# Kernel tuning notes

Measured on AMD Instinct MI355X. Metric: run time of the kernel, lower is better.

Reference implementation:

```python
import jax, jax.numpy as jnp
import numpy as np

B, H, W, P, DEPTH = 128, 512, 512, 64, 4
EPS = 1e-5


def _std(t):
    # torch.std default: unbiased (ddof=1), over last two dims, keepdim
    m = t.mean(axis=(-2, -1), keepdims=True)
    n = t.shape[-1] * t.shape[-2]
    var = ((t - m) ** 2).sum(axis=(-2, -1), keepdims=True) / (n - 1)
    return jnp.sqrt(var)


def _flat_softmax(t):
    # softmax over all non-batch dims (flatten(1).softmax(1).reshape)
    b = t.shape[0]
    return jax.nn.softmax(t.reshape(b, -1), axis=1).reshape(t.shape)


def setup_inputs() -> dict:
    key = jax.random.key(0)
    ks = jax.random.split(key, 9)
    # xavier-uniform-like scale for [*, fan_in, fan_out] params
    def init(k, shape):
        fan_in, fan_out = shape[-2], shape[-1]
        gain = float(np.sqrt(2.0))  # relu gain
        bound = gain * float(np.sqrt(6.0 / (fan_in + fan_out)))
        return jax.random.uniform(k, shape, jnp.float32, -bound, bound)
    return {
        "x": jax.random.normal(ks[0], (B, H, W), jnp.float32),
        "o_xj": init(ks[1], (DEPTH, W, P)),
        "o_xi": init(ks[2], (DEPTH, H, P)),
        "p_xj": init(ks[3], (DEPTH, H, P)),
        "p_xi": init(ks[4], (DEPTH, W, P)),
        "o_rel_xj": init(ks[5], (DEPTH, W, P)),
        "o_rel_xi": init(ks[6], (DEPTH, H, P)),
        "p_rel_xj": init(ks[7], (DEPTH, P, P)),
        "p_rel_xi": init(ks[8], (DEPTH, P, P)),
    }


def reference(x, o_xj, o_xi, p_xj, p_xi, o_rel_xj, o_rel_xi, p_rel_xj, p_rel_xi):
    # eval-mode forward (dropout inactive)
    b, h, w = x.shape
    p = o_xj.shape[-1]
    depth = o_xj.shape[0]
    scale = (h / p) * (w / p)
    x_mean = x.mean(axis=(-2, -1), keepdims=True) * scale  # [B,1,1]
    x_std = _std(x) * scale                                 # [B,1,1]
    xt = jnp.swapaxes(x, -1, -2)                            # [B,W,H]

    projection = jnp.zeros((b, p, p), jnp.float32)
    for d in range(depth):
        # relevance branches on original orientation
        o_rel_xj_sum = _flat_softmax(x @ o_rel_xj[d]).sum(axis=-2)   # [B,P]
        o_rel_xi_sum = _flat_softmax(xt @ o_rel_xi[d]).sum(axis=-2)  # [B,P]
        # projection branches
        o_t_xj = x @ o_xj[d]                                # [B,H,P]
        o_t_xi = xt @ o_xi[d]                               # [B,W,P]
        p_t_xj = jnp.swapaxes(o_t_xj, -1, -2) @ p_xj[d]     # [B,P,P]
        p_t_xi = jnp.swapaxes(o_t_xi, -1, -2) @ p_xi[d]     # [B,P,P]
        # relevance branches on permuted projection
        p_rel_xj_sum = _flat_softmax(p_t_xj @ p_rel_xj[d]).sum(axis=-2)  # [B,P]
        p_rel_xi_sum = _flat_softmax(p_t_xi @ p_rel_xi[d]).sum(axis=-2)  # [B,P]
        f_j = jnp.sqrt(o_rel_xj_sum / p_rel_xj_sum)         # [B,P]
        f_i = jnp.sqrt(o_rel_xi_sum / p_rel_xi_sum)         # [B,P]
        x_buf = p_t_xj * f_j[..., None] + jnp.swapaxes(p_t_xi * f_i[..., None], -1, -2)
        # renormalize to original (scaled) statistics
        x_buf = (x_buf - x_buf.mean(axis=(-2, -1), keepdims=True)) / (_std(x_buf) + EPS)
        x_buf = x_buf * x_std + x_mean
        projection = projection + x_buf
    return projection
```

## Files before the change

kernel.cpp:

```cpp
#include <hip/hip_runtime.h>
#include <math.h>

typedef __attribute__((ext_vector_type(8))) short short8;
typedef __attribute__((ext_vector_type(4))) short short4v;
typedef __attribute__((ext_vector_type(4))) float f32x4;

#define EPSF 1e-5f

__device__ __forceinline__ short f2bf(float f) {
    union { float f; unsigned u; } v; v.f = f;
    unsigned r = (v.u + 0x7FFFu + ((v.u >> 16) & 1u)) >> 16;
    return (short)r;
}

__device__ __forceinline__ void gload16(const void* g, void* l) {
    __builtin_amdgcn_global_load_lds(
        (const __attribute__((address_space(1))) unsigned int*)g,
        (__attribute__((address_space(3))) unsigned int*)l, 16, 0, 0);
}

__global__ __launch_bounds__(256) void prep_kernel(
    const float* __restrict__ x,
    const float* __restrict__ o_xj, const float* __restrict__ o_xi,
    const float* __restrict__ p_xj, const float* __restrict__ p_xi,
    const float* __restrict__ o_rel_xj, const float* __restrict__ o_rel_xi,
    short* __restrict__ xbf, short* __restrict__ xtbf,
    double* __restrict__ part, short* __restrict__ wcat, short* __restrict__ wpt) {
    int tid = threadIdx.x;
    if (blockIdx.x < 4096) {
        int blk = blockIdx.x;
        int b = blk >> 5, R = blk & 31;
        const float* X = x + (size_t)b * 262144 + (size_t)R * 16 * 512;
        __shared__ __align__(16) float tile[16 * 512];
        __shared__ double wsum[4][2];
        int w = tid >> 6, l = tid & 63, li = l & 15, lg = l >> 4;

        #pragma unroll
        for (int ii = 0; ii < 8; ii++) {
            int s = w * 8 + ii;
            gload16(X + s * 256 + l * 4, tile + s * 256);
        }
        __syncthreads();

        double s = 0.0, sq = 0.0;
        #pragma unroll
        for (int q = 0; q < 4; q++) {
            int kt = w * 4 + q;
            const float* p0 = tile + li * 512 + kt * 32 + lg * 8;
            float4 f0 = *(const float4*)p0;
            float4 f1 = *(const float4*)(p0 + 4);
            short v[8];
            v[0] = f2bf(f0.x); v[1] = f2bf(f0.y); v[2] = f2bf(f0.z); v[3] = f2bf(f0.w);
            v[4] = f2bf(f1.x); v[5] = f2bf(f1.y); v[6] = f2bf(f1.z); v[7] = f2bf(f1.w);
            s += (double)f0.x + (double)f0.y + (double)f0.z + (double)f0.w
               + (double)f1.x + (double)f1.y + (double)f1.z + (double)f1.w;
            sq += (double)f0.x * f0.x + (double)f0.y * f0.y + (double)f0.z * f0.z + (double)f0.w * f0.w
                + (double)f1.x * f1.x + (double)f1.y * f1.y + (double)f1.z * f1.z + (double)f1.w * f1.w;
            size_t chunk = (size_t)((b * 32 + R) * 16 + kt);
            *(short8*)(xbf + chunk * 512 + l * 8) = *(const short8*)v;
        }

        int base_lg = (R & 1) * 2;
        int kt2 = R >> 1;
        int lh = l & 31, li2 = lh & 15, lgo = lh >> 4;
        #pragma unroll
        for (int q = 0; q < 4; q++) {
            int p = w * 8 + q * 2 + (l >> 5);
            short v[8];
            #pragma unroll
            for (int e = 0; e < 8; e++)
                v[e] = f2bf(tile[(lgo * 8 + e) * 512 + p * 16 + li2]);
            size_t chunk = (size_t)((b * 32 + p) * 16 + kt2);
            *(short8*)(xtbf + chunk * 512 + (base_lg + lgo) * 128 + li2 * 8) = *(const short8*)v;
        }

        #pragma unroll
        for (int off = 1; off < 64; off <<= 1) {
            s += __shfl_xor(s, off, 64);
            sq += __shfl_xor(sq, off, 64);
        }
        if (l == 0) { wsum[w][0] = s; wsum[w][1] = sq; }
        __syncthreads();
        if (tid == 0) {
            double ts = wsum[0][0] + wsum[1][0] + wsum[2][0] + wsum[3][0];
            double tq = wsum[0][1] + wsum[1][1] + wsum[2][1] + wsum[3][1];
            part[blk * 2] = ts; part[blk * 2 + 1] = tq;
        }
    } else {
        int idx = (blockIdx.x - 4096) * 256 + tid;
        if (idx < 65536) {
            int l = idx & 63; int chunk = idx >> 6;
            int kt = chunk & 15, ns = (chunk >> 4) & 7, sd = chunk >> 7;
            int side = sd >> 2, dd = sd & 3;
            int n = ns * 16 + (l & 15);
            int k = kt * 32 + (l >> 4) * 8;
            const float* src = (n < 64) ? (side ? o_rel_xi : o_rel_xj)
                                        : (side ? o_xi : o_xj);
            src += (size_t)dd * 32768 + (n & 63);
            short8 v;
            #pragma unroll
            for (int e = 0; e < 8; e++) v[e] = f2bf(src[(size_t)(k + e) * 64]);
            *(short8*)(wcat + (size_t)chunk * 512 + l * 8) = v;
        } else {
            int j = idx - 65536;
            int l = j & 63; int chunk = j >> 6;
            int nq = chunk & 3, kk = (chunk >> 2) & 3, mt = (chunk >> 4) & 3, sd = chunk >> 6;
            int side = sd >> 2, dd = sd & 3;
            int q = nq * 16 + (l & 15);
            int r = mt * 128 + kk * 32 + (l >> 4) * 8;
            const float* src = (side ? p_xi : p_xj) + (size_t)dd * 32768 + q;
            short8 v;
            #pragma unroll
            for (int e = 0; e < 8; e++) v[e] = f2bf(src[(size_t)(r + e) * 64]);
            *(short8*)(wpt + (size_t)chunk * 512 + l * 8) = v;
        }
    }
}

__global__ __launch_bounds__(256) void stats_p1(const float* __restrict__ x,
                                                double* __restrict__ part) {
    int blk = blockIdx.x;
    const float4* X = (const float4*)(x + (size_t)blk * 65536);
    double s = 0.0, sq = 0.0;
    for (int i = threadIdx.x; i < 16384; i += 256) {
        float4 v = X[i];
        s += (double)v.x + (double)v.y + (double)v.z + (double)v.w;
        sq += (double)v.x * v.x + (double)v.y * v.y + (double)v.z * v.z + (double)v.w * v.w;
    }
    __shared__ double rs[256], rq[256];
    rs[threadIdx.x] = s; rq[threadIdx.x] = sq;
    __syncthreads();
    for (int st = 128; st > 0; st >>= 1) {
        if (threadIdx.x < st) { rs[threadIdx.x] += rs[threadIdx.x + st]; rq[threadIdx.x] += rq[threadIdx.x + st]; }
        __syncthreads();
    }
    if (threadIdx.x == 0) { part[blk * 2] = rs[0]; part[blk * 2 + 1] = rq[0]; }
}

__global__ void stats_p2(const double* __restrict__ part, float* __restrict__ stats, int ppb) {
    int b = threadIdx.x;
    double s = 0.0, sq = 0.0;
    for (int p = 0; p < ppb; p++) { s += part[(b * ppb + p) * 2]; sq += part[(b * ppb + p) * 2 + 1]; }
    double n = 262144.0;
    double mean = s / n;
    double var = (sq - n * mean * mean) / (n - 1.0);
    stats[b * 2 + 0] = (float)(mean * 64.0);
    stats[b * 2 + 1] = (float)(sqrt(var) * 64.0);
}

__global__ __launch_bounds__(256, 4) void main_mfma_kernel(
    const short* __restrict__ xbf, const short* __restrict__ xtbf,
    const short* __restrict__ wcat, const short* __restrict__ wpt,
    float* __restrict__ relsum, float* __restrict__ pt) {
    int blk = blockIdx.x;
    int xcd = blk & 7, rest = blk >> 3;
    int d = rest & 3, side = (rest >> 2) & 1, bhi = rest >> 3;
    int b = bhi * 8 + xcd;
    const short* Xsw = (side ? xtbf : xbf) + (size_t)b * 262144;
    const short* Wc  = wcat + (size_t)(side * 4 + d) * 65536;
    const short* Wp  = wpt + (size_t)(side * 4 + d) * 32768;

    __shared__ __align__(16) char lds[33792];
    short* Xs  = (short*)lds;
    short* Wsh = (short*)(lds + 8192);
    short* Tos = (short*)lds;
    short* Wps = (short*)(lds + 17408);

    int tid = threadIdx.x;
    int w = tid >> 6, l = tid & 63, li = l & 15, lg = l >> 4;
    int wm = w >> 1, wn = w & 1;

    f32x4 zero4 = {0.f, 0.f, 0.f, 0.f};
    f32x4 ptacc[4];
    #pragma unroll
    for (int i = 0; i < 4; i++) ptacc[i] = zero4;
    float esum[4] = {0.f, 0.f, 0.f, 0.f};

    for (int mt = 0; mt < 4; mt++) {
        f32x4 acc[4][4];
        #pragma unroll
        for (int i = 0; i < 4; i++)
            #pragma unroll
            for (int j = 0; j < 4; j++) acc[i][j] = zero4;

        for (int kt = 0; kt < 16; kt++) {
            __syncthreads();
            #pragma unroll
            for (int ii = 0; ii < 4; ii++) {
                int s = w * 4 + ii;
                if (s < 8)
                    gload16(Xsw + ((size_t)((mt * 8 + s) * 16 + kt)) * 512 + l * 8, Xs + s * 512);
                else
                    gload16(Wc + ((size_t)((s - 8) * 16 + kt)) * 512 + l * 8, Wsh + (s - 8) * 512);
            }
            __syncthreads();
            short8 af[4], bfv[4];
            #pragma unroll
            for (int i = 0; i < 4; i++) af[i] = *(const short8*)(Xs + (wm * 4 + i) * 512 + l * 8);
            #pragma unroll
            for (int j = 0; j < 4; j++) bfv[j] = *(const short8*)(Wsh + (wn * 4 + j) * 512 + l * 8);
            #pragma unroll
            for (int i = 0; i < 4; i++)
                #pragma unroll
                for (int j = 0; j < 4; j++)
                    acc[i][j] = __builtin_amdgcn_mfma_f32_16x16x32_bf16(af[i], bfv[j], acc[i][j], 0, 0, 0);
        }

        #pragma unroll
        for (int ii = 0; ii < 4; ii++) {
            int s = w * 4 + ii;
            gload16(Wp + ((size_t)((mt * 4 + (s >> 2)) * 4 + (s & 3))) * 512 + l * 8, Wps + s * 512);
        }
        __syncthreads();

        if (wn == 0) {
            #pragma unroll
            for (int i = 0; i < 4; i++)
                #pragma unroll
                for (int j = 0; j < 4; j++)
                    esum[j] += __expf(acc[i][j][0]) + __expf(acc[i][j][1]) +
                               __expf(acc[i][j][2]) + __expf(acc[i][j][3]);
        } else {
            #pragma unroll
            for (int i = 0; i < 4; i++)
                #pragma unroll
                for (int j = 0; j < 4; j++) {
                    int p = j * 16 + li;
                    int rb = wm * 64 + i * 16 + lg * 4;
                    short4v tv;
                    tv.x = f2bf(acc[i][j][0]); tv.y = f2bf(acc[i][j][1]);
                    tv.z = f2bf(acc[i][j][2]); tv.w = f2bf(acc[i][j][3]);
                    *(short4v*)(Tos + p * 136 + rb) = tv;
                }
        }
        __syncthreads();

        #pragma unroll
        for (int kk = 0; kk < 4; kk++) {
            short8 a = *(const short8*)(Tos + (w * 16 + li) * 136 + kk * 32 + lg * 8);
            #pragma unroll
            for (int nq = 0; nq < 4; nq++) {
                short8 bb = *(const short8*)(Wps + (kk * 4 + nq) * 512 + l * 8);
                ptacc[nq] = __builtin_amdgcn_mfma_f32_16x16x32_bf16(a, bb, ptacc[nq], 0, 0, 0);
            }
        }
    }

    __syncthreads();
    float* red = (float*)lds;
    if (wn == 0) {
        #pragma unroll
        for (int j = 0; j < 4; j++) red[wm * 256 + l * 4 + j] = esum[j];
    }
    __syncthreads();
    size_t base = (size_t)(b * 2 + side) * 4 + d;
    if (tid < 64) {
        float s = 0.f;
        #pragma unroll
        for (int w2 = 0; w2 < 2; w2++)
            #pragma unroll
            for (int g = 0; g < 4; g++)
                s += red[w2 * 256 + (g * 16 + (tid & 15)) * 4 + (tid >> 4)];
        float tot = s;
        #pragma unroll
        for (int off = 1; off < 64; off <<= 1) tot += __shfl_xor(tot, off, 64);
        relsum[base * 64 + tid] = s / tot;
    }
    float* ptout = pt + base * 4096;
    #pragma unroll
    for (int nq = 0; nq < 4; nq++)
        #pragma unroll
        for (int r = 0; r < 4; r++)
            ptout[(size_t)(w * 16 + lg * 4 + r) * 64 + nq * 16 + li] = ptacc[nq][r];
}

__global__ __launch_bounds__(256) void fused_proj_kernel(
    const float* __restrict__ x,
    const float* __restrict__ o_xj, const float* __restrict__ o_xi,
    const float* __restrict__ p_xj, const float* __restrict__ p_xi,
    const float* __restrict__ o_rel_xj, const float* __restrict__ o_rel_xi,
    float* __restrict__ relsum, float* __restrict__ pt)
{
    int blk = blockIdx.x;
    int b = blk >> 3;
    int side = (blk >> 2) & 1;
    int d = blk & 3;

    const float* Wrel = (side ? o_rel_xi : o_rel_xj) + (size_t)d * (512 * 64);
    const float* Wo   = (side ? o_xi     : o_xj)     + (size_t)d * (512 * 64);
    const float* Wp   = (side ? p_xi     : p_xj)     + (size_t)d * (512 * 64);
    const float* X = x + (size_t)b * (512 * 512);

    __shared__ float Xs[16][68];
    __shared__ float Ws[16][128];
    __shared__ float To[64][68];
    __shared__ float Wps[64][68];
    __shared__ float red[16][64];
    __shared__ float cs[64];
    __shared__ float total_s;

    int tid = threadIdx.x;
    int tx = tid & 15;
    int ty = tid >> 4;

    float paccum[4][4];
    #pragma unroll
    for (int i = 0; i < 4; i++)
        #pragma unroll
        for (int j = 0; j < 4; j++) paccum[i][j] = 0.f;
    float esum[8];
    #pragma unroll
    for (int j = 0; j < 8; j++) esum[j] = 0.f;

    for (int r0 = 0; r0 < 512; r0 += 64) {
        float acc[4][8];
        #pragma unroll
        for (int i = 0; i < 4; i++)
            #pragma unroll
            for (int j = 0; j < 8; j++) acc[i][j] = 0.f;

        for (int k0 = 0; k0 < 512; k0 += 16) {
            if (side == 0) {
                int kk = tid & 15, r = tid >> 4;
                #pragma unroll
                for (int it = 0; it < 4; it++, r += 16)
                    Xs[kk][r] = X[(size_t)(r0 + r) * 512 + (k0 + kk)];
            } else {
                int r = tid & 63, kk = tid >> 6;
                #pragma unroll
                for (int it = 0; it < 4; it++, kk += 4)
                    Xs[kk][r] = X[(size_t)(k0 + kk) * 512 + (r0 + r)];
            }
            {
                int c = tid & 127, kk = tid >> 7;
                const float* Wsrc = (c < 64) ? (Wrel + c) : (Wo + (c - 64));
                #pragma unroll
                for (int it = 0; it < 8; it++, kk += 2)
                    Ws[kk][c] = Wsrc[(size_t)(k0 + kk) * 64];
            }
            __syncthreads();
            #pragma unroll
            for (int kk = 0; kk < 16; kk++) {
                float4 a  = *(const float4*)&Xs[kk][ty * 4];
                float4 b0 = *(const float4*)&Ws[kk][tx * 8];
                float4 b1 = *(const float4*)&Ws[kk][tx * 8 + 4];
                float av[4] = {a.x, a.y, a.z, a.w};
                float bv[8] = {b0.x, b0.y, b0.z, b0.w, b1.x, b1.y, b1.z, b1.w};
                #pragma unroll
                for (int i = 0; i < 4; i++)
                    #pragma unroll
                    for (int j = 0; j < 8; j++)
                        acc[i][j] = fmaf(av[i], bv[j], acc[i][j]);
            }
            __syncthreads();
        }

        if (tx < 8) {
            #pragma unroll
            for (int i = 0; i < 4; i++)
                #pragma unroll
                for (int j = 0; j < 8; j++)
                    esum[j] += expf(acc[i][j]);
        } else {
            #pragma unroll
            for (int i = 0; i < 4; i++) {
                float4 v0 = make_float4(acc[i][0], acc[i][1], acc[i][2], acc[i][3]);
                float4 v1 = make_float4(acc[i][4], acc[i][5], acc[i][6], acc[i][7]);
                *(float4*)&To[ty * 4 + i][(tx - 8) * 8]     = v0;
                *(float4*)&To[ty * 4 + i][(tx - 8) * 8 + 4] = v1;
            }
        }
        {
            int q = tid & 63, r = tid >> 6;
            #pragma unroll
            for (int it = 0; it < 16; it++, r += 4)
                Wps[r][q] = Wp[(size_t)(r0 + r) * 64 + q];
        }
        __syncthreads();
        for (int r = 0; r < 64; r++) {
            float4 aa = *(const float4*)&To[r][ty * 4];
            float4 bb = *(const float4*)&Wps[r][tx * 4];
            float av[4] = {aa.x, aa.y, aa.z, aa.w};
            float bv[4] = {bb.x, bb.y, bb.z, bb.w};
            #pragma unroll
            for (int i = 0; i < 4; i++)
                #pragma unroll
                for (int j = 0; j < 4; j++)
                    paccum[i][j] = fmaf(av[i], bv[j], paccum[i][j]);
        }
        __syncthreads();
    }

    if (tx < 8) {
        #pragma unroll
        for (int j = 0; j < 8; j++) red[ty][tx * 8 + j] = esum[j];
    }
    __syncthreads();
    if (tid < 64) {
        float s = 0.f;
        for (int t = 0; t < 16; t++) s += red[t][tid];
        cs[tid] = s;
    }
    __syncthreads();
    if (tid == 0) {
        float tot = 0.f;
        for (int i = 0; i < 64; i++) tot += cs[i];
        total_s = tot;
    }
    __syncthreads();
    size_t base = (size_t)(b * 2 + side) * 4 + d;
    if (tid < 64) relsum[base * 64 + tid] = cs[tid] / total_s;

    float* ptout = pt + base * 4096;
    #pragma unroll
    for (int i = 0; i < 4; i++)
        #pragma unroll
        for (int j = 0; j < 4; j++)
            ptout[(size_t)(ty * 4 + i) * 64 + tx * 4 + j] = paccum[i][j];
}

__global__ __launch_bounds__(256) void finalize2_kernel(
    const float* __restrict__ relsum, const float* __restrict__ pt,
    const float* __restrict__ p_rel_xj, const float* __restrict__ p_rel_xi,
    const double* __restrict__ part, const float* __restrict__ stats, int ppb,
    float* __restrict__ out)
{
    int blk = blockIdx.x;
    int b = blk >> 2, d = blk & 3;
    int tid = threadIdx.x, tx = tid & 15, ty = tid >> 4;
    __shared__ __align__(16) float Ptj[64][68], Pti[64][68], Wr[64][68];
    __shared__ float red[16][64];
    __shared__ float fj[64], fi[64];
    __shared__ float rs[256], rq[256];
    __shared__ float bc[1];
    __shared__ float sstat[2];

    if (ppb > 0) {
        if (tid < ppb) {
            double s = part[(size_t)(b * ppb + tid) * 2];
            double sq = part[(size_t)(b * ppb + tid) * 2 + 1];
            for (int off = 1; off < ppb; off <<= 1) {
                s += __shfl_xor(s, off, 64);
                sq += __shfl_xor(sq, off, 64);
            }
            if (tid == 0) {
                double n = 262144.0;
                double mean = s / n;
                double var = (sq - n * mean * mean) / (n - 1.0);
                sstat[0] = (float)(mean * 64.0);
                sstat[1] = (float)(sqrt(var) * 64.0);
            }
        }
    } else if (tid == 0) {
        sstat[0] = stats[b * 2 + 0];
        sstat[1] = stats[b * 2 + 1];
    }

    const float* ptj = pt + ((size_t)(b * 2 + 0) * 4 + d) * 4096;
    const float* pti = pt + ((size_t)(b * 2 + 1) * 4 + d) * 4096;
    for (int it = 0; it < 16; it++) {
        int idx = tid + it * 256;
        Ptj[idx >> 6][idx & 63] = ptj[idx];
        Pti[idx >> 6][idx & 63] = pti[idx];
    }
    __syncthreads();
    float x_mean = sstat[0];
    float x_std  = sstat[1];

    for (int s = 0; s < 2; s++) {
        const float* prel = (s == 0) ? (p_rel_xj + (size_t)d * 4096)
                                     : (p_rel_xi + (size_t)d * 4096);
        for (int it = 0; it < 16; it++) {
            int idx = tid + it * 256;
            Wr[idx >> 6][idx & 63] = prel[idx];
        }
        __syncthreads();
        const float (*Pt)[68] = (s == 0) ? Ptj : Pti;
        float q[4][4];
        #pragma unroll
        for (int i = 0; i < 4; i++)
            #pragma unroll
            for (int j = 0; j < 4; j++) q[i][j] = 0.f;
        for (int r = 0; r < 64; r++) {
            float4 bv = *(const float4*)&Wr[r][tx * 4];
            #pragma unroll
            for (int i = 0; i < 4; i++) {
                float a = Pt[ty * 4 + i][r];
                q[i][0] = fmaf(a, bv.x, q[i][0]);
                q[i][1] = fmaf(a, bv.y, q[i][1]);
                q[i][2] = fmaf(a, bv.z, q[i][2]);
                q[i][3] = fmaf(a, bv.w, q[i][3]);
            }
        }
        float cpart[4];
        #pragma unroll
        for (int j = 0; j < 4; j++)
            cpart[j] = __expf(q[0][j]) + __expf(q[1][j]) + __expf(q[2][j]) + __expf(q[3][j]);
        #pragma unroll
        for (int j = 0; j < 4; j++) red[ty][tx * 4 + j] = cpart[j];
        __syncthreads();
        float* ftgt = (s == 0) ? fj : fi;
        if (tid < 64) {
            float cssum = 0.f;
            for (int t = 0; t < 16; t++) cssum += red[t][tid];
            ftgt[tid] = cssum;
        }
        __syncthreads();
        if (tid == 0) {
            float tot = 0.f;
            for (int i = 0; i < 64; i++) tot += ftgt[i];
            bc[0] = tot;
        }
        __syncthreads();
        if (tid < 64) {
            float prel_sum = ftgt[tid] / bc[0];
            float orel = relsum[((size_t)(b * 2 + s) * 4 + d) * 64 + tid];
            ftgt[tid] = sqrtf(orel / prel_sum);
        }
        __syncthreads();
    }

    float v[4][4];
    float psum = 0.f, psq = 0.f;
    #pragma unroll
    for (int i = 0; i < 4; i++) {
        int r = ty * 4 + i;
        #pragma unroll
        for (int j = 0; j < 4; j++) {
            int c = tx * 4 + j;
            float val = Ptj[r][c] * fj[r] + Pti[c][r] * fi[c];
            v[i][j] = val; psum += val; psq += val * val;
        }
    }
    rs[tid] = psum; rq[tid] = psq;
    __syncthreads();
    for (int st = 128; st > 0; st >>= 1) {
        if (tid < st) { rs[tid] += rs[tid + st]; rq[tid] += rq[tid + st]; }
        __syncthreads();
    }
    float mean = rs[0] / 4096.f;
    float var = (rq[0] - 4096.f * mean * mean) / 4095.f;
    float inv = 1.0f / (sqrtf(var) + EPSF);
    float* ob = out + (size_t)b * 4096;
    #pragma unroll
    for (int i = 0; i < 4; i++)
        #pragma unroll
        for (int j = 0; j < 4; j++)
            atomicAdd(&ob[(size_t)(ty * 4 + i) * 64 + tx * 4 + j],
                      (v[i][j] - mean) * inv * x_std + x_mean);
}

extern "C" void kernel_launch(void* const* d_in, const int* in_sizes, int n_in,
                              void* d_out, int out_size, void* d_ws, size_t ws_size,
                              hipStream_t stream) {
    const float* x        = (const float*)d_in[0];
    const float* o_xj     = (const float*)d_in[1];
    const float* o_xi     = (const float*)d_in[2];
    const float* p_xj     = (const float*)d_in[3];
    const float* p_xi     = (const float*)d_in[4];
    const float* o_rel_xj = (const float*)d_in[5];
    const float* o_rel_xi = (const float*)d_in[6];
    const float* p_rel_xj = (const float*)d_in[7];
    const float* p_rel_xi = (const float*)d_in[8];
    float* out = (float*)d_out;

    char* ws = (char*)d_ws;
    float*  stats  = (float*)(ws + 0);
    float*  relsum = (float*)(ws + 1024);
    float*  pt     = (float*)(ws + 263168);
    double* spartF = (double*)(ws + 17040384);
    short*  xbf    = (short*)(ws + 17171456);
    short*  xtbf   = (short*)(ws + 84280320);
    short*  wcat   = (short*)(ws + 151389184);
    short*  wptb   = (short*)(ws + 152437760);
    double* spartS = (double*)(ws + 17040384);

    hipMemsetAsync(d_out, 0, (size_t)out_size * sizeof(float), stream);

    const size_t FAST_NEED = 152962048;
    if (ws_size >= FAST_NEED) {
        prep_kernel<<<4480, 256, 0, stream>>>(x, o_xj, o_xi, p_xj, p_xi,
                                              o_rel_xj, o_rel_xi,
                                              xbf, xtbf, spartF, wcat, wptb);
        main_mfma_kernel<<<1024, 256, 0, stream>>>(xbf, xtbf, wcat, wptb, relsum, pt);
        finalize2_kernel<<<512, 256, 0, stream>>>(relsum, pt, p_rel_xj, p_rel_xi,
                                                  spartF, stats, 32, out);
    } else {
        if (ws_size >= 17171456) {
            stats_p1<<<512, 256, 0, stream>>>(x, spartS);
            stats_p2<<<1, 128, 0, stream>>>(spartS, stats, 4);
        } else {
            double* sp = (double*)(ws + 263168);
            stats_p1<<<512, 256, 0, stream>>>(x, sp);
            stats_p2<<<1, 128, 0, stream>>>(sp, stats, 4);
        }
        fused_proj_kernel<<<1024, 256, 0, stream>>>(x, o_xj, o_xi, p_xj, p_xi,
                                                    o_rel_xj, o_rel_xi, relsum, pt);
        finalize2_kernel<<<512, 256, 0, stream>>>(relsum, pt, p_rel_xj, p_rel_xi,
                                                  (const double*)nullptr, stats, 0, out);
    }
}
```

Measured before the change: 338.9 us.

## Split prep kernel into separate bf16-convert and transpose block groups

Splits the x-preprocessing blocks into two groups. One group reads x straight from global memory to convert it to bf16 and accumulate statistics. The other stages a tile through LDS to produce the transposed bf16 copy. The grid doubles and the per-block work is cut, aiming for more parallelism and occupancy. In exchange, x is read from global memory twice and the stats blocks use uncoalesced-ish direct loads.

```diff
diff --git a/kernel.cpp b/kernel.cpp
--- a/kernel.cpp
+++ b/kernel.cpp
@@ -26,27 +26,19 @@
     const float* __restrict__ o_rel_xj, const float* __restrict__ o_rel_xi,
     short* __restrict__ xbf, short* __restrict__ xtbf,
     double* __restrict__ part, short* __restrict__ wcat, short* __restrict__ wpt) {
+    __shared__ __align__(16) char smem[32768];
     int tid = threadIdx.x;
+    int w = tid >> 6, l = tid & 63, li = l & 15, lg = l >> 4;
+
     if (blockIdx.x < 4096) {
         int blk = blockIdx.x;
         int b = blk >> 5, R = blk & 31;
         const float* X = x + (size_t)b * 262144 + (size_t)R * 16 * 512;
-        __shared__ __align__(16) float tile[16 * 512];
-        __shared__ double wsum[4][2];
-        int w = tid >> 6, l = tid & 63, li = l & 15, lg = l >> 4;
-
-        #pragma unroll
-        for (int ii = 0; ii < 8; ii++) {
-            int s = w * 8 + ii;
-            gload16(X + s * 256 + l * 4, tile + s * 256);
-        }
-        __syncthreads();
-
         double s = 0.0, sq = 0.0;
         #pragma unroll
         for (int q = 0; q < 4; q++) {
             int kt = w * 4 + q;
-            const float* p0 = tile + li * 512 + kt * 32 + lg * 8;
+            const float* p0 = X + (size_t)li * 512 + kt * 32 + lg * 8;
             float4 f0 = *(const float4*)p0;
             float4 f1 = *(const float4*)(p0 + 4);
             short v[8];
@@ -59,7 +51,29 @@
             size_t chunk = (size_t)((b * 32 + R) * 16 + kt);
             *(short8*)(xbf + chunk * 512 + l * 8) = *(const short8*)v;
         }
-
+        #pragma unroll
+        for (int off = 1; off < 64; off <<= 1) {
+            s += __shfl_xor(s, off, 64);
+            sq += __shfl_xor(sq, off, 64);
+        }
+        double* wsum = (double*)smem;
+        if (l == 0) { wsum[w * 2] = s; wsum[w * 2 + 1] = sq; }
+        __syncthreads();
+        if (tid == 0) {
+            part[blk * 2]     = wsum[0] + wsum[2] + wsum[4] + wsum[6];
+            part[blk * 2 + 1] = wsum[1] + wsum[3] + wsum[5] + wsum[7];
+        }
+    } else if (blockIdx.x < 8192) {
+        int blk = blockIdx.x - 4096;
+        int b = blk >> 5, R = blk & 31;
+        const float* X = x + (size_t)b * 262144 + (size_t)R * 16 * 512;
+        float* tile = (float*)smem;
+        #pragma unroll
+        for (int ii = 0; ii < 8; ii++) {
+            int s = w * 8 + ii;
+            gload16(X + s * 256 + l * 4, tile + s * 256);
+        }
+        __syncthreads();
         int base_lg = (R & 1) * 2;
         int kt2 = R >> 1;
         int lh = l & 31, li2 = lh & 15, lgo = lh >> 4;
@@ -73,46 +87,33 @@
             size_t chunk = (size_t)((b * 32 + p) * 16 + kt2);
             *(short8*)(xtbf + chunk * 512 + (base_lg + lgo) * 128 + li2 * 8) = *(const short8*)v;
         }
-
-        #pragma unroll
-        for (int off = 1; off < 64; off <<= 1) {
-            s += __shfl_xor(s, off, 64);
-            sq += __shfl_xor(sq, off, 64);
-        }
-        if (l == 0) { wsum[w][0] = s; wsum[w][1] = sq; }
-        __syncthreads();
-        if (tid == 0) {
-            double ts = wsum[0][0] + wsum[1][0] + wsum[2][0] + wsum[3][0];
-            double tq = wsum[0][1] + wsum[1][1] + wsum[2][1] + wsum[3][1];
-            part[blk * 2] = ts; part[blk * 2 + 1] = tq;
-        }
     } else {
-        int idx = (blockIdx.x - 4096) * 256 + tid;
+        int idx = (blockIdx.x - 8192) * 256 + tid;
         if (idx < 65536) {
-            int l = idx & 63; int chunk = idx >> 6;
+            int ll = idx & 63; int chunk = idx >> 6;
             int kt = chunk & 15, ns = (chunk >> 4) & 7, sd = chunk >> 7;
             int side = sd >> 2, dd = sd & 3;
-            int n = ns * 16 + (l & 15);
-            int k = kt * 32 + (l >> 4) * 8;
+            int n = ns * 16 + (ll & 15);
+            int k = kt * 32 + (ll >> 4) * 8;
             const float* src = (n < 64) ? (side ? o_rel_xi : o_rel_xj)
                                         : (side ? o_xi : o_xj);
             src += (size_t)dd * 32768 + (n & 63);
             short8 v;
             #pragma unroll
             for (int e = 0; e < 8; e++) v[e] = f2bf(src[(size_t)(k + e) * 64]);
-            *(short8*)(wcat + (size_t)chunk * 512 + l * 8) = v;
+            *(short8*)(wcat + (size_t)chunk * 512 + ll * 8) = v;
         } else {
             int j = idx - 65536;
-            int l = j & 63; int chunk = j >> 6;
+            int ll = j & 63; int chunk = j >> 6;
             int nq = chunk & 3, kk = (chunk >> 2) & 3, mt = (chunk >> 4) & 3, sd = chunk >> 6;
             int side = sd >> 2, dd = sd & 3;
-            int q = nq * 16 + (l & 15);
-            int r = mt * 128 + kk * 32 + (l >> 4) * 8;
+            int q = nq * 16 + (ll & 15);
+            int r = mt * 128 + kk * 32 + (ll >> 4) * 8;
             const float* src = (side ? p_xi : p_xj) + (size_t)dd * 32768 + q;
             short8 v;
             #pragma unroll
             for (int e = 0; e < 8; e++) v[e] = f2bf(src[(size_t)(r + e) * 64]);
-            *(short8*)(wpt + (size_t)chunk * 512 + l * 8) = v;
+            *(short8*)(wpt + (size_t)chunk * 512 + ll * 8) = v;
         }
     }
 }
@@ -579,7 +580,7 @@
 
     const size_t FAST_NEED = 152962048;
     if (ws_size >= FAST_NEED) {
-        prep_kernel<<<4480, 256, 0, stream>>>(x, o_xj, o_xi, p_xj, p_xi,
+        prep_kernel<<<8576, 256, 0, stream>>>(x, o_xj, o_xi, p_xj, p_xi,
                                               o_rel_xj, o_rel_xi,
                                               xbf, xtbf, spartF, wcat, wptb);
         main_mfma_kernel<<<1024, 256, 0, stream>>>(xbf, xtbf, wcat, wptb, relsum, pt);
```

Result: slower. 361.5 us (+6.7%).
